# Performance work log

Hardware: AMD Instinct MI355X
Metric: run time of the kernel (lower is better)

The kernel has to match this reference:

```python
import jax, jax.numpy as jnp
import numpy as np

B, D, H, C = 8192, 384, 256, 6
K_MIN, K_MAX = 4, 16
LN_EPS = 1e-5


def setup_inputs() -> dict:
    key = jax.random.key(0)
    ks = jax.random.split(key, 6)
    s = lambda k, shape: (jax.random.normal(k, shape, jnp.float32) * 0.05)
    return {
        "x": jax.random.normal(ks[0], (B, D), jnp.float32),
        "W_proj": s(ks[1], (D, H)), "b_proj": jnp.zeros((H,), jnp.float32),
        "W_tau": s(ks[2], (D, 1)), "b_tau": jnp.zeros((1,), jnp.float32),
        "W_res": s(ks[3], (H, H)), "b_res": jnp.zeros((H,), jnp.float32),
        "ln_g": jnp.ones((H,), jnp.float32), "ln_b": jnp.zeros((H,), jnp.float32),
        "W_fc": s(ks[4], (H, C)), "b_fc": jnp.zeros((C,), jnp.float32),
    }


def reference(x, W_proj, b_proj, W_tau, b_tau, W_res, b_res, ln_g, ln_b, W_fc, b_fc):
    # adaptive k per sample (torch path casts to int -> non-differentiable)
    tau = jax.nn.sigmoid(x @ W_tau + b_tau)[:, 0]                      # [B]
    k = jax.lax.stop_gradient(
        jnp.clip(jnp.round(K_MAX - (K_MAX - K_MIN) * tau), 1, K_MAX)
    ).astype(jnp.int32)                                                # [B]

    # pairwise squared distances (same nearest-neighbor ordering as cdist)
    sq = jnp.sum(x * x, axis=-1)                                       # [B]
    d2 = sq[:, None] + sq[None, :] - 2.0 * (x @ x.T)                   # [B,B]
    _, idx = jax.lax.top_k(-jax.lax.stop_gradient(d2), K_MAX)          # [B,K_MAX] nearest (incl. self)

    h = jax.nn.relu(x @ W_proj + b_proj)                               # [B,H]

    # ragged top-k mean via fixed K_MAX gather + position mask
    gathered = h[idx]                                                  # [B,K_MAX,H]
    mask = (jnp.arange(K_MAX)[None, :] < k[:, None]).astype(h.dtype)   # [B,K_MAX]
    agg = jnp.einsum('bkh,bk->bh', gathered, mask) / k[:, None].astype(h.dtype)

    r = jax.nn.relu(agg @ W_res + b_res)                               # [B,H]
    z = h + r
    mu = jnp.mean(z, axis=-1, keepdims=True)
    var = jnp.var(z, axis=-1, keepdims=True)
    zn = (z - mu) / jnp.sqrt(var + LN_EPS)
    return (zn * ln_g + ln_b) @ W_fc + b_fc                            # [B,C]
```

## Files before the change

kernel.cpp:

```cpp
#include <hip/hip_runtime.h>
#include <hip/hip_fp16.h>
#include <math.h>

#define NROWS 8192
#define DDIM 384
#define HDIM 256
#define CDIM 6
#define LN_EPS 1e-5f
#define DSTR 138
#define NTILES ((NROWS/128) * (NROWS/128 + 1) / 2)
#define NGEMM1 ((NROWS/128) * (HDIM/128))
#define KSTRIDE ((size_t)NROWS * 16)

typedef short bf16x8 __attribute__((ext_vector_type(8)));
typedef float f32x4 __attribute__((ext_vector_type(4)));
typedef unsigned short u16x8 __attribute__((ext_vector_type(8)));
typedef unsigned int u32x4 __attribute__((ext_vector_type(4)));

__device__ __forceinline__ bool dj_better(float d1, int j1, float d2, int j2) {
    return (d1 < d2) || (d1 == d2 && j1 < j2);
}

__device__ __forceinline__ unsigned int umin_(unsigned int a, unsigned int b) { return a < b ? a : b; }
__device__ __forceinline__ unsigned int umax_(unsigned int a, unsigned int b) { return a > b ? a : b; }

__device__ __forceinline__ unsigned short map16f(float v) {
    union { _Float16 f; unsigned short u; } c;
    c.f = (_Float16)v;
    unsigned short b = c.u;
    return (unsigned short)(b ^ (unsigned short)((((short)b) >> 15) | 0x8000));
}

__device__ __forceinline__ float unmap16(unsigned int m16b) {
    unsigned short fb = (m16b & 0x8000u) ? (unsigned short)(m16b ^ 0x8000u)
                                         : (unsigned short)(~m16b);
    union { unsigned short u; _Float16 f; } cv; cv.u = fb;
    return (float)cv.f;
}

__device__ __forceinline__ unsigned short rne_bf16(float v) {
    unsigned int u = __float_as_uint(v);
    u += 0x7fffu + ((u >> 16) & 1u);
    return (unsigned short)(u >> 16);
}

__device__ __forceinline__ void ins8(
    unsigned int& s0, unsigned int& s1, unsigned int& s2, unsigned int& s3,
    unsigned int& s4, unsigned int& s5, unsigned int& s6, unsigned int& s7,
    unsigned int& m, unsigned int key)
{
    if (key < m) {
        s0 = (s0 == m) ? key : s0;
        s1 = (s1 == m) ? key : s1;
        s2 = (s2 == m) ? key : s2;
        s3 = (s3 == m) ? key : s3;
        s4 = (s4 == m) ? key : s4;
        s5 = (s5 == m) ? key : s5;
        s6 = (s6 == m) ? key : s6;
        s7 = (s7 == m) ? key : s7;
        m = umax_(umax_(umax_(s0, s1), umax_(s2, s3)),
                  umax_(umax_(s4, s5), umax_(s6, s7)));
    }
}

__device__ __forceinline__ unsigned int max8_(
    unsigned int s0, unsigned int s1, unsigned int s2, unsigned int s3,
    unsigned int s4, unsigned int s5, unsigned int s6, unsigned int s7)
{
    return umax_(umax_(umax_(s0, s1), umax_(s2, s3)),
                 umax_(umax_(s4, s5), umax_(s6, s7)));
}

__device__ __forceinline__ void sins8a(unsigned int (&s)[8], unsigned int key)
{
    unsigned int t = umin_(s[0], key);
    s[0] = umax_(t, s[1]); t = umin_(t, s[1]);
    s[1] = umax_(t, s[2]); t = umin_(t, s[2]);
    s[2] = umax_(t, s[3]); t = umin_(t, s[3]);
    s[3] = umax_(t, s[4]); t = umin_(t, s[4]);
    s[4] = umax_(t, s[5]); t = umin_(t, s[5]);
    s[5] = umax_(t, s[6]); t = umin_(t, s[6]);
    s[6] = umax_(t, s[7]); s[7] = umin_(t, s[7]);
}

#define CE_(a, b) { unsigned int hi_ = umax_(a, b), lo_ = umin_(a, b); a = hi_; b = lo_; }
#define SORT8A_DESC(s) \
    CE_(s[0], s[1]) CE_(s[2], s[3]) CE_(s[4], s[5]) CE_(s[6], s[7]) \
    CE_(s[0], s[2]) CE_(s[1], s[3]) CE_(s[4], s[6]) CE_(s[5], s[7]) \
    CE_(s[1], s[2]) CE_(s[5], s[6]) CE_(s[0], s[4]) CE_(s[3], s[7]) \
    CE_(s[1], s[5]) CE_(s[2], s[6]) \
    CE_(s[1], s[4]) CE_(s[3], s[6]) \
    CE_(s[2], s[4]) CE_(s[3], s[5]) \
    CE_(s[3], s[4])

__device__ __forceinline__ void scan_seed(
    const unsigned short* rowp, int cb0, unsigned int (&s)[8])
{
    u16x8 c0 = *(const u16x8*)rowp;
    s[0] = ((unsigned int)c0[0] << 13) | (unsigned int)(cb0 + 0);
    s[1] = ((unsigned int)c0[1] << 13) | (unsigned int)(cb0 + 1);
    s[2] = ((unsigned int)c0[2] << 13) | (unsigned int)(cb0 + 2);
    s[3] = ((unsigned int)c0[3] << 13) | (unsigned int)(cb0 + 3);
    s[4] = ((unsigned int)c0[4] << 13) | (unsigned int)(cb0 + 4);
    s[5] = ((unsigned int)c0[5] << 13) | (unsigned int)(cb0 + 5);
    s[6] = ((unsigned int)c0[6] << 13) | (unsigned int)(cb0 + 6);
    s[7] = ((unsigned int)c0[7] << 13) | (unsigned int)(cb0 + 7);
    SORT8A_DESC(s)
}

__device__ __forceinline__ void scan_chunk_i(
    const unsigned short* rowp, int cb0, int i, unsigned int (&s)[8])
{
    u16x8 ch = *(const u16x8*)(rowp + i * 8);
    int cb = cb0 + i * 8;
    #pragma unroll
    for (int e = 0; e < 8; ++e)
        sins8a(s, ((unsigned int)ch[e] << 13) | (unsigned int)(cb + e));
}

__device__ __forceinline__ void scan_half_dual(
    const unsigned short* rowp, int cb0, unsigned int (&SA)[8])
{
    unsigned int SB[8];
    scan_seed(rowp, cb0, SA);
    scan_seed(rowp + 8, cb0 + 8, SB);
    #pragma unroll
    for (int i = 2; i < 8; i += 2) {
        scan_chunk_i(rowp, cb0, i, SA);
        scan_chunk_i(rowp, cb0, i + 1, SB);
    }
    #pragma unroll
    for (int e = 0; e < 8; ++e) sins8a(SA, SB[e]);
}

__global__ void __launch_bounds__(256) prep_kernel(
    const float* __restrict__ x, const float* __restrict__ W_tau,
    const float* __restrict__ b_tau, unsigned short* __restrict__ xb,
    float* __restrict__ sq, int* __restrict__ kk,
    const float* __restrict__ Wp, unsigned short* __restrict__ wpT,
    const float* __restrict__ Wr, unsigned short* __restrict__ wrT)
{
    int tid = threadIdx.x;
    if (blockIdx.x < NROWS / 4) {
        int wave = tid >> 6, lane = tid & 63;
        int row = blockIdx.x * 4 + wave;
        const float* xr = x + (size_t)row * DDIM;
        unsigned short* xbr = xb + (size_t)row * DDIM;
        float s = 0.f, tp = 0.f;
        #pragma unroll
        for (int q = 0; q < 6; ++q) {
            float v = xr[lane + 64 * q];
            xbr[lane + 64 * q] = rne_bf16(v);
            s = fmaf(v, v, s);
            tp = fmaf(v, W_tau[lane + 64 * q], tp);
        }
        #pragma unroll
        for (int off = 32; off > 0; off >>= 1) {
            s += __shfl_xor(s, off);
            tp += __shfl_xor(tp, off);
        }
        if (lane == 0) {
            sq[row] = s;
            float u = tp + b_tau[0];
            float tau = 1.f / (1.f + expf(-u));
            float kf = rintf(16.f - 12.f * tau);
            int k = (int)kf;
            k = min(16, max(1, k));
            kk[row] = k;
        }
    } else {
        int i = (blockIdx.x - NROWS / 4) * 256 + tid;
        if (i < DDIM * HDIM) {
            int k = i / HDIM, n = i % HDIM;
            wpT[(size_t)n * DDIM + k] = rne_bf16(Wp[i]);
        } else {
            int j = i - DDIM * HDIM;
            if (j < HDIM * HDIM) {
                int k = j / HDIM, n = j % HDIM;
                wrT[(size_t)n * HDIM + k] = rne_bf16(Wr[j]);
            }
        }
    }
}

__device__ __forceinline__ void gemm_kloop(
    const unsigned short* __restrict__ A, const unsigned short* __restrict__ B,
    const int K, const int rowbase, const int nbase,
    unsigned short* S, f32x4 (&acc)[4][4])
{
    const int tid = threadIdx.x;
    const int wave = tid >> 6;
    const int lane = tid & 63;
    const int wr = (wave >> 1) * 64;
    const int wc = (wave & 1) * 64;
    const int m16 = lane & 15;
    const int kq = lane >> 4;
    const int er0 = tid >> 2;
    const int er1 = 64 + (tid >> 2);
    const int eko = tid & 3;
    const int NK = K >> 5;

    auto stage = [&](int kb, int set) {
        const int k0 = kb * 32;
        char* Ad = (char*)S + set * 8192;
        char* Bd = (char*)S + 16384 + set * 8192;
        __builtin_amdgcn_global_load_lds(
            (const __attribute__((address_space(1))) void*)(A + (size_t)(rowbase + er0) * K + k0 + eko * 8),
            (__attribute__((address_space(3))) void*)(Ad + (wave * 64) * 16), 16, 0, 0);
        __builtin_amdgcn_global_load_lds(
            (const __attribute__((address_space(1))) void*)(A + (size_t)(rowbase + er1) * K + k0 + eko * 8),
            (__attribute__((address_space(3))) void*)(Ad + (256 + wave * 64) * 16), 16, 0, 0);
        __builtin_amdgcn_global_load_lds(
            (const __attribute__((address_space(1))) void*)(B + (size_t)(nbase + er0) * K + k0 + eko * 8),
            (__attribute__((address_space(3))) void*)(Bd + (wave * 64) * 16), 16, 0, 0);
        __builtin_amdgcn_global_load_lds(
            (const __attribute__((address_space(1))) void*)(B + (size_t)(nbase + er1) * K + k0 + eko * 8),
            (__attribute__((address_space(3))) void*)(Bd + (256 + wave * 64) * 16), 16, 0, 0);
    };

    stage(0, 0);
    stage(1, 1);
    asm volatile("s_waitcnt vmcnt(4)" ::: "memory");
    __builtin_amdgcn_s_barrier();
    __builtin_amdgcn_sched_barrier(0);

    for (int kb = 0; kb < NK; ++kb) {
        const int cur = kb & 1;
        const unsigned short* Ab = S + cur * 4096;
        const unsigned short* Bb = S + 8192 + cur * 4096;
        bf16x8 af[4], bfr[4];
        #pragma unroll
        for (int s = 0; s < 4; ++s) {
            af[s]  = *(const bf16x8*)&Ab[(wr + s * 16 + m16) * 32 + kq * 8];
            bfr[s] = *(const bf16x8*)&Bb[(wc + s * 16 + m16) * 32 + kq * 8];
        }
        #pragma unroll
        for (int si = 0; si < 4; ++si)
            #pragma unroll
            for (int sj = 0; sj < 4; ++sj)
                acc[si][sj] = __builtin_amdgcn_mfma_f32_16x16x32_bf16(
                    af[si], bfr[sj], acc[si][sj], 0, 0, 0);
        asm volatile("s_waitcnt lgkmcnt(0)" ::: "memory");
        __builtin_amdgcn_s_barrier();
        __builtin_amdgcn_sched_barrier(0);
        if (kb + 2 < NK) {
            stage(kb + 2, cur);
            asm volatile("s_waitcnt vmcnt(4)" ::: "memory");
            __builtin_amdgcn_s_barrier();
            __builtin_amdgcn_sched_barrier(0);
        } else if (kb + 1 < NK) {
            asm volatile("s_waitcnt vmcnt(0)" ::: "memory");
            __builtin_amdgcn_s_barrier();
            __builtin_amdgcn_sched_barrier(0);
        }
    }
}

__device__ __forceinline__ void gemm_epilogue(
    const float* __restrict__ bias, float* __restrict__ out,
    unsigned short* __restrict__ hb, const int rowbase, const int nbase,
    f32x4 (&acc)[4][4])
{
    const int lane = threadIdx.x & 63;
    const int wave = threadIdx.x >> 6;
    const int wr = (wave >> 1) * 64;
    const int wc = (wave & 1) * 64;
    const int m16 = lane & 15;
    const int kq = lane >> 4;
    #pragma unroll
    for (int sj = 0; sj < 4; ++sj) {
        int c = nbase + wc + sj * 16 + m16;
        float bc = bias[c];
        #pragma unroll
        for (int si = 0; si < 4; ++si) {
            int r = rowbase + wr + si * 16 + kq * 4;
            #pragma unroll
            for (int v = 0; v < 4; ++v) {
                float val = fmaxf(acc[si][sj][v] + bc, 0.f);
                out[(size_t)(r + v) * HDIM + c] = val;
                if (hb) hb[(size_t)(r + v) * HDIM + c] = rne_bf16(val);
            }
        }
    }
}

__global__ void __launch_bounds__(256) mfma_gemm_bias_relu_kernel(
    const unsigned short* __restrict__ A, const unsigned short* __restrict__ WT,
    const float* __restrict__ bias, float* __restrict__ out,
    unsigned short* __restrict__ hb, int K)
{
    __shared__ __align__(16) unsigned short S[16384];
    f32x4 acc[4][4];
    #pragma unroll
    for (int a = 0; a < 4; ++a)
        #pragma unroll
        for (int b = 0; b < 4; ++b)
            acc[a][b] = (f32x4){0.f, 0.f, 0.f, 0.f};
    gemm_kloop(A, WT, K, blockIdx.x * 128, blockIdx.y * 128, S, acc);
    gemm_epilogue(bias, out, hb, blockIdx.x * 128, blockIdx.y * 128, acc);
}

__global__ void __launch_bounds__(256) dist_gemm_fused_kernel(
    const unsigned short* __restrict__ xb, const float* __restrict__ sq,
    unsigned int* __restrict__ keys,
    const unsigned short* __restrict__ wpT, const float* __restrict__ b_proj,
    float* __restrict__ h, unsigned short* __restrict__ hb)
{
    __shared__ __align__(16) unsigned short SMEM[128 * DSTR];

    f32x4 acc[4][4];
    #pragma unroll
    for (int a = 0; a < 4; ++a)
        #pragma unroll
        for (int b = 0; b < 4; ++b)
            acc[a][b] = (f32x4){0.f, 0.f, 0.f, 0.f};

    if (blockIdx.x < NGEMM1) {
        const int rb = (blockIdx.x >> 1) * 128;
        const int nb = (blockIdx.x & 1) * 128;
        gemm_kloop(xb, wpT, DDIM, rb, nb, SMEM, acc);
        gemm_epilogue(b_proj, h, hb, rb, nb, acc);
        return;
    }

    int t0 = blockIdx.x - NGEMM1;
    int t = (t0 & 7) * (NTILES / 8) + (t0 >> 3);
    int bi = (int)((sqrtf(8.f * (float)t + 1.f) - 1.f) * 0.5f);
    while ((bi + 1) * (bi + 2) / 2 <= t) ++bi;
    while (bi * (bi + 1) / 2 > t) --bi;
    int bj = t - bi * (bi + 1) / 2;

    const int tid = threadIdx.x;
    const int wave = tid >> 6;
    const int lane = tid & 63;
    const int rowbase = bi * 128;
    const int colbase = bj * 128;
    const int wr = (wave >> 1) * 64;
    const int wc = (wave & 1) * 64;
    const int m16 = lane & 15;
    const int kq = lane >> 4;

    gemm_kloop(xb, xb, DDIM, rowbase, colbase, SMEM, acc);
    __syncthreads();
    unsigned short* Dt = SMEM;

    const int sr = tid >> 1;
    const int seg = tid & 1;
    const unsigned short* rowp = &Dt[sr * DSTR + seg * 64];

    {
        float sqc[4];
        #pragma unroll
        for (int sj = 0; sj < 4; ++sj) sqc[sj] = sq[colbase + wc + sj * 16 + m16];
        #pragma unroll
        for (int si = 0; si < 4; ++si)
            #pragma unroll
            for (int sj = 0; sj < 4; ++sj) {
                int r = wr + si * 16 + kq * 4;
                int c = wc + sj * 16 + m16;
                #pragma unroll
                for (int v = 0; v < 4; ++v)
                    Dt[(r + v) * DSTR + c] = map16f(sqc[sj] - 2.0f * acc[si][sj][v]);
            }
        __syncthreads();

        unsigned int SA[8];
        scan_half_dual(rowp, colbase + seg * 64, SA);
        size_t kb = (size_t)bj * KSTRIDE + (size_t)(rowbase + sr) * 16 + seg * 8;
        u32x4 o0 = {SA[0], SA[1], SA[2], SA[3]};
        u32x4 o1 = {SA[4], SA[5], SA[6], SA[7]};
        __builtin_nontemporal_store(o0, (u32x4*)&keys[kb]);
        __builtin_nontemporal_store(o1, (u32x4*)&keys[kb + 4]);
    }

    if (bi != bj) {
        __syncthreads();
        #pragma unroll
        for (int si = 0; si < 4; ++si) {
            float4 sqr4 = *(const float4*)&sq[rowbase + wr + si * 16 + kq * 4];
            float srw[4] = {sqr4.x, sqr4.y, sqr4.z, sqr4.w};
            #pragma unroll
            for (int sj = 0; sj < 4; ++sj) {
                int r = wr + si * 16 + kq * 4;
                int c = wc + sj * 16 + m16;
                unsigned short h4[4];
                #pragma unroll
                for (int v = 0; v < 4; ++v)
                    h4[v] = map16f(srw[v] - 2.0f * acc[si][sj][v]);
                *(unsigned long long*)&Dt[c * DSTR + r] = *(unsigned long long*)h4;
            }
        }
        __syncthreads();

        unsigned int SA[8];
        scan_half_dual(rowp, rowbase + seg * 64, SA);
        size_t kb = (size_t)bi * KSTRIDE + (size_t)(colbase + sr) * 16 + seg * 8;
        u32x4 o0 = {SA[0], SA[1], SA[2], SA[3]};
        u32x4 o1 = {SA[4], SA[5], SA[6], SA[7]};
        __builtin_nontemporal_store(o0, (u32x4*)&keys[kb]);
        __builtin_nontemporal_store(o1, (u32x4*)&keys[kb + 4]);
    }
}

__global__ void __launch_bounds__(256) topk_rescore_agg_kernel(
    const unsigned int* __restrict__ keys, const float* __restrict__ x,
    const float* __restrict__ sq, const int* __restrict__ kk,
    const unsigned short* __restrict__ hb, unsigned short* __restrict__ aggb)
{
    const int w = threadIdx.x >> 6;
    const int row = blockIdx.x * 4 + w;
    const int lane = threadIdx.x & 63;
    __shared__ int sidx[4][16];

    const unsigned int* kpb = keys + (size_t)lane * KSTRIDE + (size_t)row * 16;
    u32x4 a0 = __builtin_nontemporal_load((const u32x4*)kpb);
    u32x4 a1 = __builtin_nontemporal_load((const u32x4*)(kpb + 4));
    unsigned int s0 = a0[0], s1 = a0[1], s2 = a0[2], s3 = a0[3];
    unsigned int s4 = a1[0], s5 = a1[1], s6 = a1[2], s7 = a1[3];
    unsigned int m = max8_(s0, s1, s2, s3, s4, s5, s6, s7);
    #pragma unroll
    for (int q = 2; q < 4; ++q) {
        u32x4 v = __builtin_nontemporal_load((const u32x4*)(kpb + q * 4));
        unsigned int gmin = umin_(umin_(v[0], v[1]), umin_(v[2], v[3]));
        if (gmin < m) {
            ins8(s0, s1, s2, s3, s4, s5, s6, s7, m, v[0]);
            ins8(s0, s1, s2, s3, s4, s5, s6, s7, m, v[1]);
            ins8(s0, s1, s2, s3, s4, s5, s6, s7, m, v[2]);
            ins8(s0, s1, s2, s3, s4, s5, s6, s7, m, v[3]);
        }
    }
    unsigned int lmin = umin_(umin_(umin_(s0, s1), umin_(s2, s3)),
                              umin_(umin_(s4, s5), umin_(s6, s7)));
    unsigned int myout = 0;
    for (int t = 0; t < 32; ++t) {
        unsigned int wv = lmin;
        #pragma unroll
        for (int off = 32; off > 0; off >>= 1)
            wv = umin_(wv, (unsigned int)__shfl_xor((int)wv, off));
        if (lane == t) myout = wv;
        if (lmin == wv) {
            s0 = (s0 == wv) ? 0xFFFFFFFFu : s0;
            s1 = (s1 == wv) ? 0xFFFFFFFFu : s1;
            s2 = (s2 == wv) ? 0xFFFFFFFFu : s2;
            s3 = (s3 == wv) ? 0xFFFFFFFFu : s3;
            s4 = (s4 == wv) ? 0xFFFFFFFFu : s4;
            s5 = (s5 == wv) ? 0xFFFFFFFFu : s5;
            s6 = (s6 == wv) ? 0xFFFFFFFFu : s6;
            s7 = (s7 == wv) ? 0xFFFFFFFFu : s7;
            lmin = umin_(umin_(umin_(s0, s1), umin_(s2, s3)),
                         umin_(umin_(s4, s5), umin_(s6, s7)));
        }
    }
    int myj = (int)(myout & 8191u);
    float dscr = (lane < 32) ? unmap16(myout >> 13) : INFINITY;

    const float EPS2 = 2.5f;
    const int k = kk[row];
    float d_k   = __shfl(dscr, k);
    float d_km1 = __shfl(dscr, k - 1);
    bool cin = false, amb = false;
    if (lane < 32) {
        if (lane < k) { cin = (dscr + EPS2 <= d_k); amb = !cin; }
        else          { amb = (dscr < d_km1 + EPS2); }
    }
    unsigned long long cinmask = __ballot(cin);
    unsigned long long ambmask = __ballot(amb);
    int n_in = __popcll(cinmask);
    int msel = k - n_in;

    float d_ex = 0.f;
    if (msel > 0) {
        float xr[6];
        #pragma unroll
        for (int q = 0; q < 6; ++q) xr[q] = x[(size_t)row * DDIM + lane + 64 * q];
        float sqrow = sq[row];
        unsigned long long mm = ambmask;
        while (mm) {
            int c = (int)(__ffsll(mm) - 1);
            mm &= mm - 1;
            int j = __shfl(myj, c);
            const float* xc = x + (size_t)j * DDIM;
            float p = 0.f;
            #pragma unroll
            for (int q = 0; q < 6; ++q) p = fmaf(xr[q], xc[lane + 64 * q], p);
            #pragma unroll
            for (int off = 32; off > 0; off >>= 1) p += __shfl_xor(p, off);
            float d = sqrow + sq[j] - 2.f * p;
            if (lane == c) d_ex = d;
        }
        int selrank = 0;
        unsigned long long mm2 = ambmask;
        while (mm2) {
            int u = (int)(__ffsll(mm2) - 1);
            mm2 &= mm2 - 1;
            float du = __shfl(d_ex, u);
            int ju = __shfl(myj, u);
            if (u != lane && dj_better(du, ju, d_ex, myj)) ++selrank;
        }
        if (amb && selrank < msel)
            sidx[w][n_in + selrank] = myj;
    }
    if (cin) {
        int pos = __popcll(cinmask & ((1ull << lane) - 1ull));
        sidx[w][pos] = myj;
    }
    __syncthreads();

    float a0f = 0.f, a1f = 0.f, a2f = 0.f, a3f = 0.f;
    for (int t = 0; t < k; ++t) {
        uint2 v = *(const uint2*)(hb + (size_t)sidx[w][t] * HDIM + lane * 4);
        a0f += __uint_as_float(v.x << 16);
        a1f += __uint_as_float(v.x & 0xFFFF0000u);
        a2f += __uint_as_float(v.y << 16);
        a3f += __uint_as_float(v.y & 0xFFFF0000u);
    }
    float inv = 1.f / (float)k;
    unsigned int b0 = rne_bf16(a0f * inv);
    unsigned int b1 = rne_bf16(a1f * inv);
    unsigned int b2 = rne_bf16(a2f * inv);
    unsigned int b3 = rne_bf16(a3f * inv);
    uint2 o; o.x = b0 | (b1 << 16); o.y = b2 | (b3 << 16);
    *(uint2*)(aggb + (size_t)row * HDIM + lane * 4) = o;
}

__global__ void __launch_bounds__(256) ln_fc_kernel(
    const float* __restrict__ h, const float* __restrict__ r,
    const float* __restrict__ g, const float* __restrict__ bb,
    const float* __restrict__ W_fc, const float* __restrict__ b_fc,
    float* __restrict__ out)
{
    const int row = blockIdx.x * 4 + (threadIdx.x >> 6);
    const int lane = threadIdx.x & 63;
    const float* hp = h + (size_t)row * HDIM;
    const float* rp = r + (size_t)row * HDIM;

    float z[4];
    #pragma unroll
    for (int q = 0; q < 4; ++q)
        z[q] = hp[lane + 64 * q] + rp[lane + 64 * q];

    float s = z[0] + z[1] + z[2] + z[3];
    float s2 = z[0]*z[0] + z[1]*z[1] + z[2]*z[2] + z[3]*z[3];
    #pragma unroll
    for (int off = 32; off > 0; off >>= 1) {
        s += __shfl_xor(s, off);
        s2 += __shfl_xor(s2, off);
    }
    float mu = s / 256.f;
    float rstd = rsqrtf(s2 / 256.f - mu * mu + LN_EPS);

    float p[6] = {0.f, 0.f, 0.f, 0.f, 0.f, 0.f};
    #pragma unroll
    for (int q = 0; q < 4; ++q) {
        int i = lane + 64 * q;
        float val = (z[q] - mu) * rstd * g[i] + bb[i];
        #pragma unroll
        for (int c = 0; c < 6; ++c)
            p[c] = fmaf(val, W_fc[i * 6 + c], p[c]);
    }
    #pragma unroll
    for (int c = 0; c < 6; ++c)
        #pragma unroll
        for (int off = 32; off > 0; off >>= 1) p[c] += __shfl_xor(p[c], off);

    if (lane < 6) {
        float o = p[0];
        o = (lane == 1) ? p[1] : o;
        o = (lane == 2) ? p[2] : o;
        o = (lane == 3) ? p[3] : o;
        o = (lane == 4) ? p[4] : o;
        o = (lane == 5) ? p[5] : o;
        out[(size_t)row * CDIM + lane] = o + b_fc[lane];
    }
}

extern "C" void kernel_launch(void* const* d_in, const int* in_sizes, int n_in,
                              void* d_out, int out_size, void* d_ws, size_t ws_size,
                              hipStream_t stream) {
    const float* x      = (const float*)d_in[0];
    const float* W_proj = (const float*)d_in[1];
    const float* b_proj = (const float*)d_in[2];
    const float* W_tau  = (const float*)d_in[3];
    const float* b_tau  = (const float*)d_in[4];
    const float* W_res  = (const float*)d_in[5];
    const float* b_res  = (const float*)d_in[6];
    const float* ln_g   = (const float*)d_in[7];
    const float* ln_b   = (const float*)d_in[8];
    const float* W_fc   = (const float*)d_in[9];
    const float* b_fc   = (const float*)d_in[10];
    float* out = (float*)d_out;

    char* ws = (char*)d_ws;
    float* sq   = (float*)ws;                        ws += (size_t)NROWS * 4;
    int*   kk   = (int*)ws;                          ws += (size_t)NROWS * 4;
    float* h    = (float*)ws;                        ws += (size_t)NROWS * HDIM * 4;
    float* r    = (float*)ws;                        ws += (size_t)NROWS * HDIM * 4;
    unsigned short* xb   = (unsigned short*)ws;      ws += (size_t)NROWS * DDIM * 2;
    unsigned short* hbuf = (unsigned short*)ws;      ws += (size_t)NROWS * HDIM * 2;
    unsigned short* aggb = (unsigned short*)ws;      ws += (size_t)NROWS * HDIM * 2;
    unsigned short* wpT  = (unsigned short*)ws;      ws += (size_t)DDIM * HDIM * 2;
    unsigned short* wrT  = (unsigned short*)ws;      ws += (size_t)HDIM * HDIM * 2;
    ws = (char*)(((size_t)ws + 255) & ~(size_t)255);
    unsigned int* keys = (unsigned int*)ws;          ws += (size_t)NROWS * 1024 * 4;

    const int prepW = (DDIM * HDIM + HDIM * HDIM + 255) / 256;
    prep_kernel<<<NROWS / 4 + prepW, 256, 0, stream>>>(
        x, W_tau, b_tau, xb, sq, kk, W_proj, wpT, W_res, wrT);
    dist_gemm_fused_kernel<<<NGEMM1 + NTILES, 256, 0, stream>>>(
        xb, sq, keys, wpT, b_proj, h, hbuf);
    topk_rescore_agg_kernel<<<NROWS / 4, 256, 0, stream>>>(keys, x, sq, kk, hbuf, aggb);
    mfma_gemm_bias_relu_kernel<<<dim3(NROWS / 128, HDIM / 128), 256, 0, stream>>>(
        aggb, wrT, b_res, r, (unsigned short*)nullptr, HDIM);
    ln_fc_kernel<<<NROWS / 4, 256, 0, stream>>>(h, r, ln_g, ln_b, W_fc, b_fc, out);
}
```

Before: 231.9 us.

## Enlarge distance and projection GEMM tiles to 256x256 with 512-thread blocks

Switches the fused distance/projection GEMM and the residual GEMM from 128x128 tiles with 256 threads to 256x256 tiles with 512 threads. Each wave now computes 64x128 outputs, and the top-k scan over the distance tile runs in two 128-row passes through doubled LDS. This cuts global and LDS reloads per output and halves the tile count, but it raises register pressure (64 accumulators per wave), LDS use, and barriers. Fewer blocks can also leave CUs idle, especially for the 32-block projection GEMMs.

```diff
diff --git a/kernel.cpp b/kernel.cpp
--- a/kernel.cpp
+++ b/kernel.cpp
@@ -8,8 +8,8 @@
 #define CDIM 6
 #define LN_EPS 1e-5f
 #define DSTR 138
-#define NTILES ((NROWS/128) * (NROWS/128 + 1) / 2)
-#define NGEMM1 ((NROWS/128) * (HDIM/128))
+#define NT256 ((NROWS/256) * (NROWS/256 + 1) / 2)
+#define NG1 (NROWS/256)
 #define KSTRIDE ((size_t)NROWS * 16)
 
 typedef short bf16x8 __attribute__((ext_vector_type(8)));
@@ -133,6 +133,16 @@
     for (int e = 0; e < 8; ++e) sins8a(SA, SB[e]);
 }
 
+__device__ __forceinline__ void scan_store(
+    const unsigned int (&SA)[8], unsigned int* __restrict__ keys, int row, int g64)
+{
+    size_t kb = (size_t)(g64 >> 1) * KSTRIDE + (size_t)row * 16 + (size_t)(g64 & 1) * 8;
+    u32x4 o0 = {SA[0], SA[1], SA[2], SA[3]};
+    u32x4 o1 = {SA[4], SA[5], SA[6], SA[7]};
+    __builtin_nontemporal_store(o0, (u32x4*)&keys[kb]);
+    __builtin_nontemporal_store(o1, (u32x4*)&keys[kb + 4]);
+}
+
 __global__ void __launch_bounds__(256) prep_kernel(
     const float* __restrict__ x, const float* __restrict__ W_tau,
     const float* __restrict__ b_tau, unsigned short* __restrict__ xb,
@@ -183,39 +193,38 @@
     }
 }
 
-__device__ __forceinline__ void gemm_kloop(
+__device__ __forceinline__ void kloop512(
     const unsigned short* __restrict__ A, const unsigned short* __restrict__ B,
     const int K, const int rowbase, const int nbase,
-    unsigned short* S, f32x4 (&acc)[4][4])
+    unsigned short* S, f32x4 (&acc)[4][8])
 {
     const int tid = threadIdx.x;
     const int wave = tid >> 6;
     const int lane = tid & 63;
     const int wr = (wave >> 1) * 64;
-    const int wc = (wave & 1) * 64;
+    const int wc = (wave & 1) * 128;
     const int m16 = lane & 15;
     const int kq = lane >> 4;
     const int er0 = tid >> 2;
-    const int er1 = 64 + (tid >> 2);
     const int eko = tid & 3;
     const int NK = K >> 5;
 
     auto stage = [&](int kb, int set) {
         const int k0 = kb * 32;
-        char* Ad = (char*)S + set * 8192;
-        char* Bd = (char*)S + 16384 + set * 8192;
+        char* Ad = (char*)S + set * 16384;
+        char* Bd = (char*)S + 32768 + set * 16384;
         __builtin_amdgcn_global_load_lds(
             (const __attribute__((address_space(1))) void*)(A + (size_t)(rowbase + er0) * K + k0 + eko * 8),
-            (__attribute__((address_space(3))) void*)(Ad + (wave * 64) * 16), 16, 0, 0);
+            (__attribute__((address_space(3))) void*)(Ad + wave * 1024), 16, 0, 0);
         __builtin_amdgcn_global_load_lds(
-            (const __attribute__((address_space(1))) void*)(A + (size_t)(rowbase + er1) * K + k0 + eko * 8),
-            (__attribute__((address_space(3))) void*)(Ad + (256 + wave * 64) * 16), 16, 0, 0);
+            (const __attribute__((address_space(1))) void*)(A + (size_t)(rowbase + 128 + er0) * K + k0 + eko * 8),
+            (__attribute__((address_space(3))) void*)(Ad + 8192 + wave * 1024), 16, 0, 0);
         __builtin_amdgcn_global_load_lds(
             (const __attribute__((address_space(1))) void*)(B + (size_t)(nbase + er0) * K + k0 + eko * 8),
-            (__attribute__((address_space(3))) void*)(Bd + (wave * 64) * 16), 16, 0, 0);
+            (__attribute__((address_space(3))) void*)(Bd + wave * 1024), 16, 0, 0);
         __builtin_amdgcn_global_load_lds(
-            (const __attribute__((address_space(1))) void*)(B + (size_t)(nbase + er1) * K + k0 + eko * 8),
-            (__attribute__((address_space(3))) void*)(Bd + (256 + wave * 64) * 16), 16, 0, 0);
+            (const __attribute__((address_space(1))) void*)(B + (size_t)(nbase + 128 + er0) * K + k0 + eko * 8),
+            (__attribute__((address_space(3))) void*)(Bd + 8192 + wave * 1024), 16, 0, 0);
     };
 
     stage(0, 0);
@@ -226,20 +235,21 @@
 
     for (int kb = 0; kb < NK; ++kb) {
         const int cur = kb & 1;
-        const unsigned short* Ab = S + cur * 4096;
-        const unsigned short* Bb = S + 8192 + cur * 4096;
-        bf16x8 af[4], bfr[4];
-        #pragma unroll
-        for (int s = 0; s < 4; ++s) {
-            af[s]  = *(const bf16x8*)&Ab[(wr + s * 16 + m16) * 32 + kq * 8];
-            bfr[s] = *(const bf16x8*)&Bb[(wc + s * 16 + m16) * 32 + kq * 8];
-        }
+        const unsigned short* Ab = S + cur * 8192;
+        const unsigned short* Bb = S + 16384 + cur * 8192;
+        bf16x8 af[4], bfr[8];
+        #pragma unroll
+        for (int s = 0; s < 4; ++s)
+            af[s] = *(const bf16x8*)&Ab[(wr + s * 16 + m16) * 32 + kq * 8];
+        #pragma unroll
+        for (int n = 0; n < 8; ++n)
+            bfr[n] = *(const bf16x8*)&Bb[(wc + n * 16 + m16) * 32 + kq * 8];
         #pragma unroll
         for (int si = 0; si < 4; ++si)
             #pragma unroll
-            for (int sj = 0; sj < 4; ++sj)
-                acc[si][sj] = __builtin_amdgcn_mfma_f32_16x16x32_bf16(
-                    af[si], bfr[sj], acc[si][sj], 0, 0, 0);
+            for (int nj = 0; nj < 8; ++nj)
+                acc[si][nj] = __builtin_amdgcn_mfma_f32_16x16x32_bf16(
+                    af[si], bfr[nj], acc[si][nj], 0, 0, 0);
         asm volatile("s_waitcnt lgkmcnt(0)" ::: "memory");
         __builtin_amdgcn_s_barrier();
         __builtin_amdgcn_sched_barrier(0);
@@ -256,27 +266,27 @@
     }
 }
 
-__device__ __forceinline__ void gemm_epilogue(
+__device__ __forceinline__ void epi512(
     const float* __restrict__ bias, float* __restrict__ out,
     unsigned short* __restrict__ hb, const int rowbase, const int nbase,
-    f32x4 (&acc)[4][4])
+    f32x4 (&acc)[4][8])
 {
     const int lane = threadIdx.x & 63;
     const int wave = threadIdx.x >> 6;
     const int wr = (wave >> 1) * 64;
-    const int wc = (wave & 1) * 64;
+    const int wc = (wave & 1) * 128;
     const int m16 = lane & 15;
     const int kq = lane >> 4;
     #pragma unroll
-    for (int sj = 0; sj < 4; ++sj) {
-        int c = nbase + wc + sj * 16 + m16;
+    for (int nj = 0; nj < 8; ++nj) {
+        int c = nbase + wc + nj * 16 + m16;
         float bc = bias[c];
         #pragma unroll
         for (int si = 0; si < 4; ++si) {
             int r = rowbase + wr + si * 16 + kq * 4;
             #pragma unroll
             for (int v = 0; v < 4; ++v) {
-                float val = fmaxf(acc[si][sj][v] + bc, 0.f);
+                float val = fmaxf(acc[si][nj][v] + bc, 0.f);
                 out[(size_t)(r + v) * HDIM + c] = val;
                 if (hb) hb[(size_t)(r + v) * HDIM + c] = rne_bf16(val);
             }
@@ -284,47 +294,46 @@
     }
 }
 
-__global__ void __launch_bounds__(256) mfma_gemm_bias_relu_kernel(
+__global__ void __launch_bounds__(512) mfma_gemm512_kernel(
     const unsigned short* __restrict__ A, const unsigned short* __restrict__ WT,
     const float* __restrict__ bias, float* __restrict__ out,
     unsigned short* __restrict__ hb, int K)
 {
-    __shared__ __align__(16) unsigned short S[16384];
-    f32x4 acc[4][4];
+    __shared__ __align__(16) unsigned short S[32768];
+    f32x4 acc[4][8];
     #pragma unroll
     for (int a = 0; a < 4; ++a)
         #pragma unroll
-        for (int b = 0; b < 4; ++b)
+        for (int b = 0; b < 8; ++b)
             acc[a][b] = (f32x4){0.f, 0.f, 0.f, 0.f};
-    gemm_kloop(A, WT, K, blockIdx.x * 128, blockIdx.y * 128, S, acc);
-    gemm_epilogue(bias, out, hb, blockIdx.x * 128, blockIdx.y * 128, acc);
-}
-
-__global__ void __launch_bounds__(256) dist_gemm_fused_kernel(
+    kloop512(A, WT, K, blockIdx.x * 256, 0, S, acc);
+    epi512(bias, out, hb, blockIdx.x * 256, 0, acc);
+}
+
+__global__ void __launch_bounds__(512) dist_gemm_fused_kernel(
     const unsigned short* __restrict__ xb, const float* __restrict__ sq,
     unsigned int* __restrict__ keys,
     const unsigned short* __restrict__ wpT, const float* __restrict__ b_proj,
     float* __restrict__ h, unsigned short* __restrict__ hb)
 {
-    __shared__ __align__(16) unsigned short SMEM[128 * DSTR];
-
-    f32x4 acc[4][4];
+    __shared__ __align__(16) unsigned short SMEM[2 * 128 * DSTR];
+
+    f32x4 acc[4][8];
     #pragma unroll
     for (int a = 0; a < 4; ++a)
         #pragma unroll
-        for (int b = 0; b < 4; ++b)
+        for (int b = 0; b < 8; ++b)
             acc[a][b] = (f32x4){0.f, 0.f, 0.f, 0.f};
 
-    if (blockIdx.x < NGEMM1) {
-        const int rb = (blockIdx.x >> 1) * 128;
-        const int nb = (blockIdx.x & 1) * 128;
-        gemm_kloop(xb, wpT, DDIM, rb, nb, SMEM, acc);
-        gemm_epilogue(b_proj, h, hb, rb, nb, acc);
+    if (blockIdx.x < NG1) {
+        const int rb = blockIdx.x * 256;
+        kloop512(xb, wpT, DDIM, rb, 0, SMEM, acc);
+        epi512(b_proj, h, hb, rb, 0, acc);
         return;
     }
 
-    int t0 = blockIdx.x - NGEMM1;
-    int t = (t0 & 7) * (NTILES / 8) + (t0 >> 3);
+    int t0 = blockIdx.x - NG1;
+    int t = (t0 & 7) * (NT256 / 8) + (t0 >> 3);
     int bi = (int)((sqrtf(8.f * (float)t + 1.f) - 1.f) * 0.5f);
     while ((bi + 1) * (bi + 2) / 2 <= t) ++bi;
     while (bi * (bi + 1) / 2 > t) --bi;
@@ -333,72 +342,81 @@
     const int tid = threadIdx.x;
     const int wave = tid >> 6;
     const int lane = tid & 63;
-    const int rowbase = bi * 128;
-    const int colbase = bj * 128;
-    const int wr = (wave >> 1) * 64;
-    const int wc = (wave & 1) * 64;
+    const int rowbase = bi * 256;
+    const int colbase = bj * 256;
     const int m16 = lane & 15;
     const int kq = lane >> 4;
 
-    gemm_kloop(xb, xb, DDIM, rowbase, colbase, SMEM, acc);
+    kloop512(xb, xb, DDIM, rowbase, colbase, SMEM, acc);
     __syncthreads();
-    unsigned short* Dt = SMEM;
-
-    const int sr = tid >> 1;
-    const int seg = tid & 1;
-    const unsigned short* rowp = &Dt[sr * DSTR + seg * 64];
-
-    {
-        float sqc[4];
-        #pragma unroll
-        for (int sj = 0; sj < 4; ++sj) sqc[sj] = sq[colbase + wc + sj * 16 + m16];
-        #pragma unroll
-        for (int si = 0; si < 4; ++si)
+
+    unsigned short* DtA = SMEM;
+    unsigned short* DtB = SMEM + 128 * DSTR;
+
+    const int hb128 = (tid >= 256);
+    const int t2 = tid & 255;
+    const int sr = t2 >> 1;
+    const int seg = t2 & 1;
+    const unsigned short* rowp = (hb128 ? DtB : DtA) + sr * DSTR + seg * 64;
+
+    const int whalf = wave & 1;
+    const int wslab = wave >> 2;
+    const int rl0 = ((wave >> 1) & 1) * 64;
+    unsigned short* myDt = whalf ? DtB : DtA;
+
+    #pragma unroll
+    for (int s = 0; s < 2; ++s) {
+        if (wslab == s) {
+            float sqc[8];
             #pragma unroll
-            for (int sj = 0; sj < 4; ++sj) {
-                int r = wr + si * 16 + kq * 4;
-                int c = wc + sj * 16 + m16;
+            for (int nj = 0; nj < 8; ++nj)
+                sqc[nj] = sq[colbase + whalf * 128 + nj * 16 + m16];
+            #pragma unroll
+            for (int si = 0; si < 4; ++si)
                 #pragma unroll
-                for (int v = 0; v < 4; ++v)
-                    Dt[(r + v) * DSTR + c] = map16f(sqc[sj] - 2.0f * acc[si][sj][v]);
+                for (int nj = 0; nj < 8; ++nj) {
+                    int r = rl0 + si * 16 + kq * 4;
+                    int c = nj * 16 + m16;
+                    #pragma unroll
+                    for (int v = 0; v < 4; ++v)
+                        myDt[(r + v) * DSTR + c] = map16f(sqc[nj] - 2.0f * acc[si][nj][v]);
+                }
+        }
+        __syncthreads();
+        unsigned int SA[8];
+        scan_half_dual(rowp, colbase + hb128 * 128 + seg * 64, SA);
+        scan_store(SA, keys, rowbase + s * 128 + sr,
+                   (colbase >> 6) + hb128 * 2 + seg);
+        __syncthreads();
+    }
+
+    if (bi != bj) {
+        #pragma unroll
+        for (int u = 0; u < 2; ++u) {
+            if (wslab == u) {
+                #pragma unroll
+                for (int si = 0; si < 4; ++si) {
+                    float4 sqr4 = *(const float4*)&sq[rowbase + u * 128 + rl0 + si * 16 + kq * 4];
+                    float srw[4] = {sqr4.x, sqr4.y, sqr4.z, sqr4.w};
+                    #pragma unroll
+                    for (int nj = 0; nj < 8; ++nj) {
+                        int cl = nj * 16 + m16;
+                        int rl = rl0 + si * 16 + kq * 4;
+                        unsigned short h4[4];
+                        #pragma unroll
+                        for (int v = 0; v < 4; ++v)
+                            h4[v] = map16f(srw[v] - 2.0f * acc[si][nj][v]);
+                        *(unsigned long long*)&myDt[cl * DSTR + rl] = *(unsigned long long*)h4;
+                    }
+                }
             }
-        __syncthreads();
-
-        unsigned int SA[8];
-        scan_half_dual(rowp, colbase + seg * 64, SA);
-        size_t kb = (size_t)bj * KSTRIDE + (size_t)(rowbase + sr) * 16 + seg * 8;
-        u32x4 o0 = {SA[0], SA[1], SA[2], SA[3]};
-        u32x4 o1 = {SA[4], SA[5], SA[6], SA[7]};
-        __builtin_nontemporal_store(o0, (u32x4*)&keys[kb]);
-        __builtin_nontemporal_store(o1, (u32x4*)&keys[kb + 4]);
-    }
-
-    if (bi != bj) {
-        __syncthreads();
-        #pragma unroll
-        for (int si = 0; si < 4; ++si) {
-            float4 sqr4 = *(const float4*)&sq[rowbase + wr + si * 16 + kq * 4];
-            float srw[4] = {sqr4.x, sqr4.y, sqr4.z, sqr4.w};
-            #pragma unroll
-            for (int sj = 0; sj < 4; ++sj) {
-                int r = wr + si * 16 + kq * 4;
-                int c = wc + sj * 16 + m16;
-                unsigned short h4[4];
-                #pragma unroll
-                for (int v = 0; v < 4; ++v)
-                    h4[v] = map16f(srw[v] - 2.0f * acc[si][sj][v]);
-                *(unsigned long long*)&Dt[c * DSTR + r] = *(unsigned long long*)h4;
-            }
-        }
-        __syncthreads();
-
-        unsigned int SA[8];
-        scan_half_dual(rowp, rowbase + seg * 64, SA);
-        size_t kb = (size_t)bi * KSTRIDE + (size_t)(colbase + sr) * 16 + seg * 8;
-        u32x4 o0 = {SA[0], SA[1], SA[2], SA[3]};
-        u32x4 o1 = {SA[4], SA[5], SA[6], SA[7]};
-        __builtin_nontemporal_store(o0, (u32x4*)&keys[kb]);
-        __builtin_nontemporal_store(o1, (u32x4*)&keys[kb + 4]);
+            __syncthreads();
+            unsigned int SA[8];
+            scan_half_dual(rowp, rowbase + u * 128 + seg * 64, SA);
+            scan_store(SA, keys, colbase + hb128 * 128 + sr,
+                       (rowbase >> 6) + u * 2 + seg);
+            __syncthreads();
+        }
     }
 }
 
@@ -606,10 +624,10 @@
     const int prepW = (DDIM * HDIM + HDIM * HDIM + 255) / 256;
     prep_kernel<<<NROWS / 4 + prepW, 256, 0, stream>>>(
         x, W_tau, b_tau, xb, sq, kk, W_proj, wpT, W_res, wrT);
-    dist_gemm_fused_kernel<<<NGEMM1 + NTILES, 256, 0, stream>>>(
+    dist_gemm_fused_kernel<<<NG1 + NT256, 512, 0, stream>>>(
         xb, sq, keys, wpT, b_proj, h, hbuf);
     topk_rescore_agg_kernel<<<NROWS / 4, 256, 0, stream>>>(keys, x, sq, kk, hbuf, aggb);
-    mfma_gemm_bias_relu_kernel<<<dim3(NROWS / 128, HDIM / 128), 256, 0, stream>>>(
+    mfma_gemm512_kernel<<<NROWS / 256, 512, 0, stream>>>(
         aggb, wrT, b_res, r, (unsigned short*)nullptr, HDIM);
     ln_fc_kernel<<<NROWS / 4, 256, 0, stream>>>(h, r, ln_g, ln_b, W_fc, b_fc, out);
 }
```

New measurement: 262.7 us. 1.13x slower.

## Fuse residual GEMM with LayerNorm and FC head; drop nontemporal key traffic

Applied to the files above, without the earlier changes.

Replaces the separate W_res GEMM and LN+FC kernels with one kernel. Each block computes a 64x256 row tile via MFMA with double-buffered LDS loads, then applies bias+relu, the residual add, LayerNorm and the 6-wide projection in registers. This removes one launch and the write and re-read of the fp32 r buffer. Separately, the key buffer stores and loads switch from nontemporal to ordinary accesses so the keys can stay in cache between kernels. The cost is only 128 blocks for the fused kernel and higher register pressure from holding 16 accumulators plus per-column constants.

```diff
diff --git a/kernel.cpp b/kernel.cpp
--- a/kernel.cpp
+++ b/kernel.cpp
@@ -284,22 +284,6 @@
     }
 }
 
-__global__ void __launch_bounds__(256) mfma_gemm_bias_relu_kernel(
-    const unsigned short* __restrict__ A, const unsigned short* __restrict__ WT,
-    const float* __restrict__ bias, float* __restrict__ out,
-    unsigned short* __restrict__ hb, int K)
-{
-    __shared__ __align__(16) unsigned short S[16384];
-    f32x4 acc[4][4];
-    #pragma unroll
-    for (int a = 0; a < 4; ++a)
-        #pragma unroll
-        for (int b = 0; b < 4; ++b)
-            acc[a][b] = (f32x4){0.f, 0.f, 0.f, 0.f};
-    gemm_kloop(A, WT, K, blockIdx.x * 128, blockIdx.y * 128, S, acc);
-    gemm_epilogue(bias, out, hb, blockIdx.x * 128, blockIdx.y * 128, acc);
-}
-
 __global__ void __launch_bounds__(256) dist_gemm_fused_kernel(
     const unsigned short* __restrict__ xb, const float* __restrict__ sq,
     unsigned int* __restrict__ keys,
@@ -367,10 +351,10 @@
         unsigned int SA[8];
         scan_half_dual(rowp, colbase + seg * 64, SA);
         size_t kb = (size_t)bj * KSTRIDE + (size_t)(rowbase + sr) * 16 + seg * 8;
-        u32x4 o0 = {SA[0], SA[1], SA[2], SA[3]};
-        u32x4 o1 = {SA[4], SA[5], SA[6], SA[7]};
-        __builtin_nontemporal_store(o0, (u32x4*)&keys[kb]);
-        __builtin_nontemporal_store(o1, (u32x4*)&keys[kb + 4]);
+        uint4 o0; o0.x = SA[0]; o0.y = SA[1]; o0.z = SA[2]; o0.w = SA[3];
+        uint4 o1; o1.x = SA[4]; o1.y = SA[5]; o1.z = SA[6]; o1.w = SA[7];
+        *(uint4*)&keys[kb] = o0;
+        *(uint4*)&keys[kb + 4] = o1;
     }
 
     if (bi != bj) {
@@ -395,10 +379,10 @@
         unsigned int SA[8];
         scan_half_dual(rowp, rowbase + seg * 64, SA);
         size_t kb = (size_t)bi * KSTRIDE + (size_t)(colbase + sr) * 16 + seg * 8;
-        u32x4 o0 = {SA[0], SA[1], SA[2], SA[3]};
-        u32x4 o1 = {SA[4], SA[5], SA[6], SA[7]};
-        __builtin_nontemporal_store(o0, (u32x4*)&keys[kb]);
-        __builtin_nontemporal_store(o1, (u32x4*)&keys[kb + 4]);
+        uint4 o0; o0.x = SA[0]; o0.y = SA[1]; o0.z = SA[2]; o0.w = SA[3];
+        uint4 o1; o1.x = SA[4]; o1.y = SA[5]; o1.z = SA[6]; o1.w = SA[7];
+        *(uint4*)&keys[kb] = o0;
+        *(uint4*)&keys[kb + 4] = o1;
     }
 }
 
@@ -413,14 +397,14 @@
     __shared__ int sidx[4][16];
 
     const unsigned int* kpb = keys + (size_t)lane * KSTRIDE + (size_t)row * 16;
-    u32x4 a0 = __builtin_nontemporal_load((const u32x4*)kpb);
-    u32x4 a1 = __builtin_nontemporal_load((const u32x4*)(kpb + 4));
+    u32x4 a0 = *(const u32x4*)kpb;
+    u32x4 a1 = *(const u32x4*)(kpb + 4);
     unsigned int s0 = a0[0], s1 = a0[1], s2 = a0[2], s3 = a0[3];
     unsigned int s4 = a1[0], s5 = a1[1], s6 = a1[2], s7 = a1[3];
     unsigned int m = max8_(s0, s1, s2, s3, s4, s5, s6, s7);
     #pragma unroll
     for (int q = 2; q < 4; ++q) {
-        u32x4 v = __builtin_nontemporal_load((const u32x4*)(kpb + q * 4));
+        u32x4 v = *(const u32x4*)(kpb + q * 4);
         unsigned int gmin = umin_(umin_(v[0], v[1]), umin_(v[2], v[3]));
         if (gmin < m) {
             ins8(s0, s1, s2, s3, s4, s5, s6, s7, m, v[0]);
@@ -523,54 +507,115 @@
     *(uint2*)(aggb + (size_t)row * HDIM + lane * 4) = o;
 }
 
-__global__ void __launch_bounds__(256) ln_fc_kernel(
-    const float* __restrict__ h, const float* __restrict__ r,
-    const float* __restrict__ g, const float* __restrict__ bb,
+__global__ void __launch_bounds__(256) res_ln_fc_kernel(
+    const unsigned short* __restrict__ aggb, const unsigned short* __restrict__ wrT,
+    const float* __restrict__ b_res, const float* __restrict__ h,
+    const float* __restrict__ ln_g, const float* __restrict__ ln_b,
     const float* __restrict__ W_fc, const float* __restrict__ b_fc,
     float* __restrict__ out)
 {
-    const int row = blockIdx.x * 4 + (threadIdx.x >> 6);
-    const int lane = threadIdx.x & 63;
-    const float* hp = h + (size_t)row * HDIM;
-    const float* rp = r + (size_t)row * HDIM;
-
-    float z[4];
-    #pragma unroll
-    for (int q = 0; q < 4; ++q)
-        z[q] = hp[lane + 64 * q] + rp[lane + 64 * q];
-
-    float s = z[0] + z[1] + z[2] + z[3];
-    float s2 = z[0]*z[0] + z[1]*z[1] + z[2]*z[2] + z[3]*z[3];
-    #pragma unroll
-    for (int off = 32; off > 0; off >>= 1) {
-        s += __shfl_xor(s, off);
-        s2 += __shfl_xor(s2, off);
-    }
-    float mu = s / 256.f;
-    float rstd = rsqrtf(s2 / 256.f - mu * mu + LN_EPS);
-
-    float p[6] = {0.f, 0.f, 0.f, 0.f, 0.f, 0.f};
-    #pragma unroll
-    for (int q = 0; q < 4; ++q) {
-        int i = lane + 64 * q;
-        float val = (z[q] - mu) * rstd * g[i] + bb[i];
-        #pragma unroll
-        for (int c = 0; c < 6; ++c)
-            p[c] = fmaf(val, W_fc[i * 6 + c], p[c]);
-    }
-    #pragma unroll
-    for (int c = 0; c < 6; ++c)
-        #pragma unroll
-        for (int off = 32; off > 0; off >>= 1) p[c] += __shfl_xor(p[c], off);
-
-    if (lane < 6) {
-        float o = p[0];
-        o = (lane == 1) ? p[1] : o;
-        o = (lane == 2) ? p[2] : o;
-        o = (lane == 3) ? p[3] : o;
-        o = (lane == 4) ? p[4] : o;
-        o = (lane == 5) ? p[5] : o;
-        out[(size_t)row * CDIM + lane] = o + b_fc[lane];
+    __shared__ __align__(16) unsigned short S[20480];
+    const int tid = threadIdx.x;
+    const int wave = tid >> 6;
+    const int lane = tid & 63;
+    const int m16 = lane & 15;
+    const int kq = lane >> 4;
+    const int rb = blockIdx.x * 64;
+
+    f32x4 acc[16];
+    #pragma unroll
+    for (int n = 0; n < 16; ++n) acc[n] = (f32x4){0.f, 0.f, 0.f, 0.f};
+
+    auto stage = [&](int kb, int set) {
+        const int k0 = kb * 32;
+        char* Ad = (char*)S + set * 20480;
+        char* Bd = (char*)S + set * 20480 + 4096;
+        __builtin_amdgcn_global_load_lds(
+            (const __attribute__((address_space(1))) void*)(aggb + (size_t)(rb + (tid >> 2)) * HDIM + k0 + (tid & 3) * 8),
+            (__attribute__((address_space(3))) void*)(Ad + wave * 1024), 16, 0, 0);
+        #pragma unroll
+        for (int n0 = 0; n0 < 256; n0 += 64)
+            __builtin_amdgcn_global_load_lds(
+                (const __attribute__((address_space(1))) void*)(wrT + (size_t)(n0 + (tid >> 2)) * HDIM + k0 + (tid & 3) * 8),
+                (__attribute__((address_space(3))) void*)(Bd + n0 * 64 + wave * 1024), 16, 0, 0);
+    };
+
+    stage(0, 0);
+    __syncthreads();
+    for (int kb = 0; kb < HDIM / 32; ++kb) {
+        const int cur = kb & 1;
+        if (kb + 1 < HDIM / 32) stage(kb + 1, cur ^ 1);
+        const unsigned short* Ab = S + cur * 10240;
+        const unsigned short* Bb = S + cur * 10240 + 2048;
+        bf16x8 af = *(const bf16x8*)&Ab[(wave * 16 + m16) * 32 + kq * 8];
+        #pragma unroll
+        for (int nj = 0; nj < 16; ++nj) {
+            bf16x8 bf_ = *(const bf16x8*)&Bb[(nj * 16 + m16) * 32 + kq * 8];
+            acc[nj] = __builtin_amdgcn_mfma_f32_16x16x32_bf16(af, bf_, acc[nj], 0, 0, 0);
+        }
+        __syncthreads();
+    }
+
+    float gr[16], br[16], bres[16], wf[16][6];
+    #pragma unroll
+    for (int nj = 0; nj < 16; ++nj) {
+        int col = nj * 16 + m16;
+        gr[nj] = ln_g[col];
+        br[nj] = ln_b[col];
+        bres[nj] = b_res[col];
+        #pragma unroll
+        for (int c = 0; c < 6; ++c) wf[nj][c] = W_fc[col * 6 + c];
+    }
+    const float bfc = (m16 < 6) ? b_fc[m16] : 0.f;
+
+    #pragma unroll
+    for (int v = 0; v < 4; ++v) {
+        const int row = rb + wave * 16 + kq * 4 + v;
+        const float* hrow = h + (size_t)row * HDIM;
+        float z[16];
+        float s = 0.f, s2 = 0.f;
+        #pragma unroll
+        for (int nj = 0; nj < 16; ++nj) {
+            float r_ = fmaxf(acc[nj][v] + bres[nj], 0.f);
+            float zz = hrow[nj * 16 + m16] + r_;
+            z[nj] = zz;
+            s += zz;
+            s2 = fmaf(zz, zz, s2);
+        }
+        #pragma unroll
+        for (int off = 8; off > 0; off >>= 1) {
+            s += __shfl_xor(s, off);
+            s2 += __shfl_xor(s2, off);
+        }
+        float mu = s * (1.f / 256.f);
+        float rstd = rsqrtf(s2 * (1.f / 256.f) - mu * mu + LN_EPS);
+        float p0 = 0.f, p1 = 0.f, p2 = 0.f, p3 = 0.f, p4 = 0.f, p5 = 0.f;
+        #pragma unroll
+        for (int nj = 0; nj < 16; ++nj) {
+            float zn = (z[nj] - mu) * rstd * gr[nj] + br[nj];
+            p0 = fmaf(zn, wf[nj][0], p0);
+            p1 = fmaf(zn, wf[nj][1], p1);
+            p2 = fmaf(zn, wf[nj][2], p2);
+            p3 = fmaf(zn, wf[nj][3], p3);
+            p4 = fmaf(zn, wf[nj][4], p4);
+            p5 = fmaf(zn, wf[nj][5], p5);
+        }
+        #pragma unroll
+        for (int off = 8; off > 0; off >>= 1) {
+            p0 += __shfl_xor(p0, off);
+            p1 += __shfl_xor(p1, off);
+            p2 += __shfl_xor(p2, off);
+            p3 += __shfl_xor(p3, off);
+            p4 += __shfl_xor(p4, off);
+            p5 += __shfl_xor(p5, off);
+        }
+        float o = p0;
+        o = (m16 == 1) ? p1 : o;
+        o = (m16 == 2) ? p2 : o;
+        o = (m16 == 3) ? p3 : o;
+        o = (m16 == 4) ? p4 : o;
+        o = (m16 == 5) ? p5 : o;
+        if (m16 < 6) out[(size_t)row * CDIM + m16] = o + bfc;
     }
 }
 
@@ -594,7 +639,6 @@
     float* sq   = (float*)ws;                        ws += (size_t)NROWS * 4;
     int*   kk   = (int*)ws;                          ws += (size_t)NROWS * 4;
     float* h    = (float*)ws;                        ws += (size_t)NROWS * HDIM * 4;
-    float* r    = (float*)ws;                        ws += (size_t)NROWS * HDIM * 4;
     unsigned short* xb   = (unsigned short*)ws;      ws += (size_t)NROWS * DDIM * 2;
     unsigned short* hbuf = (unsigned short*)ws;      ws += (size_t)NROWS * HDIM * 2;
     unsigned short* aggb = (unsigned short*)ws;      ws += (size_t)NROWS * HDIM * 2;
@@ -609,7 +653,6 @@
     dist_gemm_fused_kernel<<<NGEMM1 + NTILES, 256, 0, stream>>>(
         xb, sq, keys, wpT, b_proj, h, hbuf);
     topk_rescore_agg_kernel<<<NROWS / 4, 256, 0, stream>>>(keys, x, sq, kk, hbuf, aggb);
-    mfma_gemm_bias_relu_kernel<<<dim3(NROWS / 128, HDIM / 128), 256, 0, stream>>>(
-        aggb, wrT, b_res, r, (unsigned short*)nullptr, HDIM);
-    ln_fc_kernel<<<NROWS / 4, 256, 0, stream>>>(h, r, ln_g, ln_b, W_fc, b_fc, out);
-}
+    res_ln_fc_kernel<<<NROWS / 64, 256, 0, stream>>>(
+        aggb, wrT, b_res, h, ln_g, ln_b, W_fc, b_fc, out);
+}
```

Result: faster. 223.2 us (-3.8%).
